# Kernel tuning notes

Measured on AMD Instinct MI355X. Metric: run time of the kernel, lower is better.

Reference implementation:

```python
import jax, jax.numpy as jnp
import numpy as np

B, T = 16, 8192
L, RC, DC, SC, EC, E, NC = 16, 32, 32, 256, 256, 100, 256


def conv1d(x, w, b, dilation=1):
    # x: [B, Cin, T], w: [Cout, Cin, K], b: [Cout]
    y = jax.lax.conv_general_dilated(
        x, w, window_strides=(1,), padding='VALID',
        rhs_dilation=(dilation,), dimension_numbers=('NCH', 'OIH', 'NCH'))
    return y + b[None, :, None]


def setup_inputs() -> dict:
    key = jax.random.key(0)
    ks = jax.random.split(key, 32)
    n = lambda k, shp: (jax.random.normal(k, shp) * 0.1).astype(jnp.float32)
    return dict(
        tokens=jax.random.randint(ks[0], (B, T), 0, NC),
        emb=n(ks[1], (NC, E)),
        init_w=n(ks[2], (RC, E, 1)), init_b=n(ks[3], (RC,)),
        dil_w=n(ks[4], (L, DC, RC, 2)), dil_b=n(ks[5], (L, DC)),
        filt_w=n(ks[6], (L, DC, DC, 2)), filt_b=n(ks[7], (L, DC)),
        gate_w=n(ks[8], (L, DC, DC, 2)), gate_b=n(ks[9], (L, DC)),
        res_w=n(ks[10], (L, RC, DC, 1)), res_b=n(ks[11], (L, RC)),
        skip_w=n(ks[12], (L, SC, DC, 1)), skip_b=n(ks[13], (L, SC)),
        end1_w=n(ks[14], (EC, SC, 1)), end1_b=n(ks[15], (EC,)),
        end2_w=n(ks[16], (EC, EC, 1)), end2_b=n(ks[17], (EC,)),
        fc1_w=n(ks[18], (128, 256)), fc1_b=n(ks[19], (128,)),
        fc2_w=n(ks[20], (128, 128)), fc2_b=n(ks[21], (128,)),
        fc3_w=n(ks[22], (64, 128)), fc3_b=n(ks[23], (64,)),
        fc4_w=n(ks[24], (NC, 64)), fc4_b=n(ks[25], (NC,)),
    )


def reference(tokens, emb, init_w, init_b, dil_w, dil_b, filt_w, filt_b,
              gate_w, gate_b, res_w, res_b, skip_w, skip_b,
              end1_w, end1_b, end2_w, end2_b,
              fc1_w, fc1_b, fc2_w, fc2_b, fc3_w, fc3_b, fc4_w, fc4_b):
    x = emb[tokens]                     # [B, T, E]
    x = jnp.transpose(x, (0, 2, 1))     # [B, E, T]
    x = conv1d(x, init_w, init_b)       # [B, RC, T]
    skip = None
    for i in range(L):
        d = 2 ** (i % 4)                # dilation resets each block of 4 layers
        xp = jnp.pad(x, ((0, 0), (0, 0), (d + 1, 0)))        # left pad d+1
        residual = conv1d(xp, dil_w[i], dil_b[i], dilation=d)  # [B, DC, T+1]
        f = jnp.tanh(conv1d(residual, filt_w[i], filt_b[i]))   # [B, DC, T]
        g = jax.nn.sigmoid(conv1d(residual, gate_w[i], gate_b[i]))
        x = f * g
        skip = conv1d(x, skip_w[i], skip_b[i])   # overwritten each layer (source bug, kept faithful)
        x = conv1d(x, res_w[i], res_b[i]) + residual[:, :, :-1]
    h = jax.nn.relu(conv1d(jax.nn.relu(skip), end1_w, end1_b))
    h = conv1d(h, end2_w, end2_b)       # [B, EC, T]
    h = h[:, :, -1]                     # [B, 256] last timestep only
    h = jax.nn.relu(h @ fc1_w.T + fc1_b)
    h = jax.nn.relu(h @ fc2_w.T + fc2_b)
    h = jax.nn.relu(h @ fc3_w.T + fc3_b)
    out = h @ fc4_w.T + fc4_b           # [B, NC]
    return out
```

## Files before the change

### kernel.cpp

```cpp
#include <hip/hip_runtime.h>


#define BB 16
#define TT 8192
#define LL 16
#define W0 77
#define NT 256

typedef __attribute__((ext_vector_type(8)))  short short8;
typedef __attribute__((ext_vector_type(16))) float float16;

#define MFMA_B16(a, b, c) __builtin_amdgcn_mfma_f32_32x32x16_bf16(a, b, c, 0, 0, 0)

__device__ __forceinline__ short f2bs(float f) {
  union { float ff; unsigned u; } v; v.ff = f;
  unsigned u = v.u;
  return (short)((u + 0x7FFFu + ((u >> 16) & 1u)) >> 16);
}
__device__ __forceinline__ float b2f(short h) {
  union { unsigned u; float f; } v;
  v.u = ((unsigned)(unsigned short)h) << 16; return v.f;
}
__device__ __forceinline__ unsigned cvtpk(float lo, float hi) {
  unsigned r;
  asm("v_cvt_pk_bf16_f32 %0, %1, %2" : "=v"(r) : "v"(lo), "v"(hi));
  return r;
}
__device__ __forceinline__ short8 mk8(unsigned a, unsigned b, unsigned c, unsigned d) {
  union { unsigned u[4]; short8 s; } z;
  z.u[0] = a; z.u[1] = b; z.u[2] = c; z.u[3] = d; return z.s;
}
__device__ __forceinline__ float u2f(unsigned u) {
  union { unsigned x; float f; } z; z.x = u; return z.f;
}
__device__ __forceinline__ void asmb(const unsigned* own, const unsigned* cr,
                                     int kh, unsigned* o) {
  #pragma unroll
  for (int h = 0; h < 2; h++) {
    o[4*h+0] = kh ? cr[4*h+2] : own[4*h+0];
    o[4*h+1] = kh ? cr[4*h+3] : own[4*h+1];
    o[4*h+2] = kh ? own[4*h+2] : cr[4*h+0];
    o[4*h+3] = kh ? own[4*h+3] : cr[4*h+1];
  }
}

__device__ __forceinline__ void afrag2(const short* src, int row, int kh, short8* out) {
  out[0] = *(const short8*)&src[row * 32 + 8 * kh];
  out[1] = *(const short8*)&src[row * 32 + 16 + 8 * kh];
}

__device__ __forceinline__ void ldrow(const short* xb, int row, int kh, unsigned* w8) {
  #pragma unroll
  for (int h = 0; h < 2; h++) {
    short8 v = *(const short8*)&xb[row * 32 + 16 * h + 8 * kh];
    union { short8 s; unsigned u[4]; } z; z.s = v;
    #pragma unroll
    for (int s = 0; s < 4; s++) w8[4 * h + s] = z.u[s];
  }
}

__device__ __forceinline__ void load_chunk(
    int li, int cid, float* pf,
    const float* dil_w, const float* filt_w, const float* gate_w, const float* res_w)
{
  int mat = cid >> 7;
  int h = (cid >> 6) & 1, ln = cid & 63;
  int n = ln & 31, k2 = ln >> 5;
  int base = (li * 32 + n) * 32 + 16 * h + 8 * k2;
  if (mat == 6) {
    const float* p = res_w + base;
    #pragma unroll
    for (int j = 0; j < 8; j++) pf[j] = p[j];
  } else {
    const float* w = (mat < 2) ? dil_w : (mat < 4) ? filt_w : gate_w;
    const float* p = w + base * 2 + (mat & 1);
    #pragma unroll
    for (int j = 0; j < 8; j++) pf[j] = p[2 * j];
  }
}

__global__ __launch_bounds__(NT, 1) void wavenet_kernel(
    const int* __restrict__ tokens,
    const float* __restrict__ emb,
    const float* __restrict__ init_w, const float* __restrict__ init_b,
    const float* __restrict__ dil_w,  const float* __restrict__ dil_b,
    const float* __restrict__ filt_w, const float* __restrict__ filt_b,
    const float* __restrict__ gate_w, const float* __restrict__ gate_b,
    const float* __restrict__ res_w,  const float* __restrict__ res_b,
    const float* __restrict__ skip_w, const float* __restrict__ skip_b,
    const float* __restrict__ end1_w, const float* __restrict__ end1_b,
    const float* __restrict__ end2_w, const float* __restrict__ end2_b,
    const float* __restrict__ fc1_w,  const float* __restrict__ fc1_b,
    const float* __restrict__ fc2_w,  const float* __restrict__ fc2_b,
    const float* __restrict__ fc3_w,  const float* __restrict__ fc3_b,
    const float* __restrict__ fc4_w,  const float* __restrict__ fc4_b,
    float* __restrict__ out)
{
  __shared__ __align__(16) short bfw[2][7168];
  __shared__ __align__(16) float bias2[2][128];
  __shared__ __align__(16) short xbuf[2][W0 * 32];
  __shared__ __align__(16) short pool[8624];
  __shared__ int tok[W0];
  __shared__ __align__(16) float vecA[256], vecB[256];

  short* rb = pool;
  short* xm = pool + 2432;

  const int tid  = threadIdx.x;
  const int lane = tid & 63;
  const int wv   = tid >> 6;
  const int m    = lane & 31;
  const int kh   = lane >> 5;
  const int b    = blockIdx.x;

  if (tid < W0) tok[tid] = tokens[b * TT + (TT - 1 - tid)];
  __syncthreads();

  for (int cid = tid; cid < 77 * 14; cid += NT) {
    int u = cid / 14, s = cid % 14;
    const float* er = emb + tok[u] * 100 + s * 8;
    short8 v;
    if (s < 12) {
      #pragma unroll
      for (int j = 0; j < 8; j++) v[j] = f2bs(er[j]);
    } else if (s == 12) {
      #pragma unroll
      for (int j = 0; j < 4; j++) v[j] = f2bs(er[j]);
      #pragma unroll
      for (int j = 4; j < 8; j++) v[j] = 0;
    } else {
      #pragma unroll
      for (int j = 0; j < 8; j++) v[j] = 0;
    }
    *(short8*)&pool[u * 112 + s * 8] = v;
  }
  for (int cid = tid; cid < 896; cid += NT) {
    float pf[8];
    load_chunk(0, cid, pf, dil_w, filt_w, gate_w, res_w);
    short8 v;
    #pragma unroll
    for (int j = 0; j < 8; j++) v[j] = f2bs(pf[j]);
    *(short8*)&bfw[0][cid * 8] = v;
  }
  if (tid < 128) {
    const float* bsrc = (tid < 32) ? dil_b : (tid < 64) ? filt_b : (tid < 96) ? gate_b : res_b;
    bias2[0][tid] = bsrc[tid & 31];
  }
  __syncthreads();

  if (wv < 3) {
    short8 bi[7];
    #pragma unroll
    for (int s = 0; s < 7; s++) {
      const float* p = init_w + m * 100 + s * 16 + kh * 8;
      short8 v;
      if (s < 6) {
        #pragma unroll
        for (int j = 0; j < 8; j++) v[j] = f2bs(p[j]);
      } else if (kh == 0) {
        #pragma unroll
        for (int j = 0; j < 4; j++) v[j] = f2bs(p[j]);
        #pragma unroll
        for (int j = 4; j < 8; j++) v[j] = 0;
      } else {
        #pragma unroll
        for (int j = 0; j < 8; j++) v[j] = 0;
      }
      bi[s] = v;
    }
    const float binit = init_b[m];
    const int R = wv * 32;
    int u = R + m; if (u > 76) u = 76;
    float16 acc;
    #pragma unroll
    for (int r = 0; r < 16; r++) acc[r] = binit;
    #pragma unroll
    for (int s = 0; s < 7; s++) {
      short8 a = *(const short8*)&pool[u * 112 + s * 16 + kh * 8];
      acc = MFMA_B16(a, bi[s], acc);
    }
    #pragma unroll
    for (int r = 0; r < 16; r++) {
      int row = (r & 3) + 8 * (r >> 2) + 4 * kh;
      int uu = R + row;
      if (uu < W0) xbuf[0][uu * 32 + m] = f2bs(acc[r]);
    }
  }
  __syncthreads();

  int Win = W0;
  for (int i = 0; i < 10; i++) {
    const int d = 1 << (i & 3);
    const int Wout = Win - d - 1;
    const int T = (Wout + 31) / 31;
    const short* bw = bfw[i & 1];
    const float* bs = bias2[i & 1];
    const short* xin  = xbuf[i & 1];
    short* xout = xbuf[(i + 1) & 1];

    float pfo[4][8];
    float pbias = 0.f;
    const int nch = (tid < 128) ? 4 : 3;
    const bool oldpf = (T >= 3) && (i + 1 < LL);
    if (oldpf) {
      #pragma unroll
      for (int q = 0; q < 4; q++) {
        if (q < nch)
          load_chunk(i + 1, tid + q * NT, pfo[q], dil_w, filt_w, gate_w, res_w);
      }
      if (tid < 128) {
        const float* bsrc = (tid < 32) ? dil_b : (tid < 64) ? filt_b : (tid < 96) ? gate_b : res_b;
        pbias = bsrc[(i + 1) * 32 + (tid & 31)];
      }
    }
    const bool newpf = (T <= 2) && (i + 1 < LL) && (wv >= T);
    const int nP = NT - T * 64;
    const int ptid = tid - T * 64;
    float pfn[7][8];
    if (newpf) {
      #pragma unroll
      for (int q = 0; q < 7; q++) {
        int c = ptid + q * nP;
        if (c < 896) load_chunk(i + 1, c, pfn[q], dil_w, filt_w, gate_w, res_w);
      }
    }

    if (wv < T) {
      const int R = wv * 31;
      short8 B0[2], B1[2], BW[5][2];
      #pragma unroll
      for (int h = 0; h < 2; h++) {
        B0[h] = *(const short8*)&bw[((0 * 2 + h) * 64 + lane) * 8];
        B1[h] = *(const short8*)&bw[((1 * 2 + h) * 64 + lane) * 8];
      }
      #pragma unroll
      for (int mt = 0; mt < 5; mt++)
        #pragma unroll
        for (int h = 0; h < 2; h++)
          BW[mt][h] = *(const short8*)&bw[(((mt + 2) * 2 + h) * 64 + lane) * 8];

      int vra = R + m + d; if (vra > Win - 1) vra = Win - 1;
      int vrz = R + m;     if (vrz > Win - 1) vrz = Win - 1;
      short8 aA[2], aZ[2];
      afrag2(xin, vra, kh, aA);
      afrag2(xin, vrz, kh, aZ);
      float16 acc;
      const float bc = bs[m];
      #pragma unroll
      for (int r = 0; r < 16; r++) acc[r] = bc;
      acc = MFMA_B16(aA[0], B0[0], acc);
      acc = MFMA_B16(aA[1], B0[1], acc);
      acc = MFMA_B16(aZ[0], B1[0], acc);
      acc = MFMA_B16(aZ[1], B1[1], acc);
      #pragma unroll
      for (int r = 0; r < 16; r++) {
        int row = (r & 3) + 8 * (r >> 2) + 4 * kh;
        int vr = R + row;
        if (vr <= Wout) rb[vr * 32 + m] = f2bs(acc[r]);
      }
      asm volatile("s_waitcnt lgkmcnt(0)" ::: "memory");

      const int capA = (R + 31 < Wout) ? (R + 31) : Wout;
      int r1 = R + m + 1; if (r1 > capA) r1 = capA;
      int r0 = R + m;     if (r0 > Wout) r0 = Wout;
      short8 a1[2], a0[2];
      afrag2(rb, r1, kh, a1);
      afrag2(rb, r0, kh, a0);
      float16 accF, accG;
      const float bf = bs[32 + m], bg = bs[64 + m];
      #pragma unroll
      for (int r = 0; r < 16; r++) { accF[r] = bf; accG[r] = bg; }
      accF = MFMA_B16(a1[0], BW[0][0], accF);
      accF = MFMA_B16(a1[1], BW[0][1], accF);
      accF = MFMA_B16(a0[0], BW[1][0], accF);
      accF = MFMA_B16(a0[1], BW[1][1], accF);
      accG = MFMA_B16(a1[0], BW[2][0], accG);
      accG = MFMA_B16(a1[1], BW[2][1], accG);
      accG = MFMA_B16(a0[0], BW[3][0], accG);
      accG = MFMA_B16(a0[1], BW[3][1], accG);
      #pragma unroll
      for (int r = 0; r < 16; r++) {
        int row = (r & 3) + 8 * (r >> 2) + 4 * kh;
        int uf = R + row;
        if (row < 31 && uf < Wout) {
          float u = __expf(-2.f * accF[r]);
          float v = __expf(-accG[r]);
          float fg = (1.f - u) * __builtin_amdgcn_rcpf((1.f + u) * (1.f + v));
          xm[uf * 32 + m] = f2bs(fg);
        }
      }
      asm volatile("s_waitcnt lgkmcnt(0)" ::: "memory");

      const int capX = (R + 30 < Wout - 1) ? (R + 30) : (Wout - 1);
      int rx = R + m; if (rx > capX) rx = capX;
      short8 aX[2];
      afrag2(xm, rx, kh, aX);
      float16 accX;
      const float br = bs[96 + m];
      #pragma unroll
      for (int r = 0; r < 16; r++) {
        int row = (r & 3) + 8 * (r >> 2) + 4 * kh;
        int rr = R + row + 1; if (rr > Wout) rr = Wout;
        accX[r] = br + b2f(rb[rr * 32 + m]);
      }
      accX = MFMA_B16(aX[0], BW[4][0], accX);
      accX = MFMA_B16(aX[1], BW[4][1], accX);
      #pragma unroll
      for (int r = 0; r < 16; r++) {
        int row = (r & 3) + 8 * (r >> 2) + 4 * kh;
        int uf = R + row;
        if (row < 31 && uf < Wout) xout[uf * 32 + m] = f2bs(accX[r]);
      }
    } else if (newpf) {
      short* dst = bfw[(i + 1) & 1];
      #pragma unroll
      for (int q = 0; q < 7; q++) {
        int c = ptid + q * nP;
        if (c < 896) {
          short8 v;
          #pragma unroll
          for (int j = 0; j < 8; j++) v[j] = f2bs(pfn[q][j]);
          *(short8*)&dst[c * 8] = v;
        }
      }
      for (int t2 = ptid; t2 < 128; t2 += nP) {
        const float* bsrc = (t2 < 32) ? dil_b : (t2 < 64) ? filt_b : (t2 < 96) ? gate_b : res_b;
        bias2[(i + 1) & 1][t2] = bsrc[(i + 1) * 32 + (t2 & 31)];
      }
    }

    if (oldpf) {
      short* dst = bfw[(i + 1) & 1];
      #pragma unroll
      for (int q = 0; q < 4; q++) {
        if (q < nch) {
          short8 v;
          #pragma unroll
          for (int j = 0; j < 8; j++) v[j] = f2bs(pfo[q][j]);
          *(short8*)&dst[(tid + q * NT) * 8] = v;
        }
      }
      if (tid < 128) bias2[(i + 1) & 1][tid] = pbias;
    }
    __syncthreads();
    Win = Wout;
  }

  {
    const int t31 = lane & 31;
    const int hb  = lane & 32;
    unsigned xcur[8], e32[8], e33[8];
    if (wv == 0) {
      const short* xb0 = xbuf[0];
      int tcl = t31 < Win - 1 ? t31 : Win - 1;
      ldrow(xb0, tcl, kh, xcur);
      ldrow(xb0, 32, kh, e32);
      ldrow(xb0, 33, kh, e33);
    }

    #pragma unroll
    for (int i = 10; i < LL; i++) {
      const int d = 1 << (i & 3);
      const int Wout = Win - d - 1;
      const short* bw = bfw[i & 1];
      const float* bs = bias2[i & 1];

      const bool npf = (i + 1 < LL) && (wv >= 1);
      const int ptid = tid - 64;
      float pfn[7][8];
      if (npf) {
        #pragma unroll
        for (int q = 0; q < 7; q++) {
          int c = ptid + q * 192;
          if (c < 896) load_chunk(i + 1, c, pfn[q], dil_w, filt_w, gate_w, res_w);
        }
      }

      if (wv == 0) {
        short8 WA[7][2];
        #pragma unroll
        for (int mt = 0; mt < 7; mt++)
          #pragma unroll
          for (int h = 0; h < 2; h++)
            WA[mt][h] = *(const short8*)&bw[((mt * 2 + h) * 64 + lane) * 8];

        unsigned xd[8];
        if (i == 10) {
          int td = t31 + d;
          int ts = td > 31 ? 31 : td;
          #pragma unroll
          for (int q = 0; q < 8; q++) {
            unsigned s = (unsigned)__shfl((int)xcur[q], hb | ts);
            s = (td == 32) ? e32[q] : s;
            s = (td >= 33) ? e33[q] : s;
            xd[q] = s;
          }
        } else {
          int td = t31 + d; if (td > Win - 1) td = Win - 1;
          int srcd = hb | td;
          #pragma unroll
          for (int q = 0; q < 8; q++) xd[q] = (unsigned)__shfl((int)xcur[q], srcd);
        }
        float16 acc;
        #pragma unroll
        for (int g = 0; g < 4; g++) {
          float4 b4 = *(const float4*)&bs[4 * kh + 8 * g];
          acc[4*g+0] = b4.x; acc[4*g+1] = b4.y; acc[4*g+2] = b4.z; acc[4*g+3] = b4.w;
        }
        acc = MFMA_B16(WA[0][0], mk8(xd[0], xd[1], xd[2], xd[3]), acc);
        acc = MFMA_B16(WA[0][1], mk8(xd[4], xd[5], xd[6], xd[7]), acc);
        acc = MFMA_B16(WA[1][0], mk8(xcur[0], xcur[1], xcur[2], xcur[3]), acc);
        acc = MFMA_B16(WA[1][1], mk8(xcur[4], xcur[5], xcur[6], xcur[7]), acc);

        unsigned wrb[8], xc[8], x1[8], x1c[8];
        #pragma unroll
        for (int q = 0; q < 8; q++) wrb[q] = cvtpk(acc[2 * q], acc[2 * q + 1]);
        int t1 = t31 + 1; if (t1 > Wout) t1 = Wout;
        int s1o = hb | t1;
        int s1c = (hb ^ 32) | t1;
        #pragma unroll
        for (int q = 0; q < 8; q++) {
          xc[q]  = (unsigned)__shfl((int)wrb[q], lane ^ 32);
          x1[q]  = (unsigned)__shfl((int)wrb[q], s1o);
          x1c[q] = (unsigned)__shfl((int)wrb[q], s1c);
        }
        unsigned rb0w[8], rb1w[8];
        asmb(wrb, xc, kh, rb0w);
        asmb(x1, x1c, kh, rb1w);

        float16 accF, accG;
        #pragma unroll
        for (int g = 0; g < 4; g++) {
          float4 bF = *(const float4*)&bs[32 + 4 * kh + 8 * g];
          float4 bG = *(const float4*)&bs[64 + 4 * kh + 8 * g];
          accF[4*g+0] = bF.x; accF[4*g+1] = bF.y; accF[4*g+2] = bF.z; accF[4*g+3] = bF.w;
          accG[4*g+0] = bG.x; accG[4*g+1] = bG.y; accG[4*g+2] = bG.z; accG[4*g+3] = bG.w;
        }
        short8 RB10 = mk8(rb1w[0], rb1w[1], rb1w[2], rb1w[3]);
        short8 RB11 = mk8(rb1w[4], rb1w[5], rb1w[6], rb1w[7]);
        short8 RB00 = mk8(rb0w[0], rb0w[1], rb0w[2], rb0w[3]);
        short8 RB01 = mk8(rb0w[4], rb0w[5], rb0w[6], rb0w[7]);
        accF = MFMA_B16(WA[2][0], RB10, accF);
        accF = MFMA_B16(WA[2][1], RB11, accF);
        accF = MFMA_B16(WA[3][0], RB00, accF);
        accF = MFMA_B16(WA[3][1], RB01, accF);
        accG = MFMA_B16(WA[4][0], RB10, accG);
        accG = MFMA_B16(WA[4][1], RB11, accG);
        accG = MFMA_B16(WA[5][0], RB00, accG);
        accG = MFMA_B16(WA[5][1], RB01, accG);
        float fg[16];
        #pragma unroll
        for (int r = 0; r < 16; r++) {
          float u = __expf(-2.f * accF[r]);
          float v = __expf(-accG[r]);
          fg[r] = (1.f - u) * __builtin_amdgcn_rcpf((1.f + u) * (1.f + v));
        }
        unsigned wxm[8];
        #pragma unroll
        for (int q = 0; q < 8; q++) wxm[q] = cvtpk(fg[2 * q], fg[2 * q + 1]);

        if (i == LL - 1) {
          if (t31 == 0) {
            #pragma unroll
            for (int q = 0; q < 8; q++) {
              int c0 = (2 * q & 3) + 8 * (q >> 1) + 4 * kh;
              *(unsigned*)&xm[c0] = wxm[q];
            }
          }
        } else {
          unsigned xmc[8];
          #pragma unroll
          for (int q = 0; q < 8; q++) xmc[q] = (unsigned)__shfl((int)wxm[q], lane ^ 32);
          unsigned xmw[8];
          asmb(wxm, xmc, kh, xmw);
          float16 accX;
          #pragma unroll
          for (int g = 0; g < 4; g++) {
            float4 bR = *(const float4*)&bs[96 + 4 * kh + 8 * g];
            #pragma unroll
            for (int j = 0; j < 4; j++) {
              int r = 4 * g + j;
              unsigned w = x1[r >> 1];
              float rv = (r & 1) ? u2f(w & 0xFFFF0000u) : u2f(w << 16);
              accX[r] = ((const float*)&bR)[j] + rv;
            }
          }
          accX = MFMA_B16(WA[6][0], mk8(xmw[0], xmw[1], xmw[2], xmw[3]), accX);
          accX = MFMA_B16(WA[6][1], mk8(xmw[4], xmw[5], xmw[6], xmw[7]), accX);
          unsigned wxn[8], xnc[8];
          #pragma unroll
          for (int q = 0; q < 8; q++) wxn[q] = cvtpk(accX[2 * q], accX[2 * q + 1]);
          #pragma unroll
          for (int q = 0; q < 8; q++) xnc[q] = (unsigned)__shfl((int)wxn[q], lane ^ 32);
          asmb(wxn, xnc, kh, xcur);
        }
      } else if (npf) {
        short* dst = bfw[(i + 1) & 1];
        #pragma unroll
        for (int q = 0; q < 7; q++) {
          int c = ptid + q * 192;
          if (c < 896) {
            short8 v;
            #pragma unroll
            for (int j = 0; j < 8; j++) v[j] = f2bs(pfn[q][j]);
            *(short8*)&dst[c * 8] = v;
          }
        }
        for (int t2 = ptid; t2 < 128; t2 += 192) {
          const float* bsrc = (t2 < 32) ? dil_b : (t2 < 64) ? filt_b : (t2 < 96) ? gate_b : res_b;
          bias2[(i + 1) & 1][t2] = bsrc[(i + 1) * 32 + (t2 & 31)];
        }
      }
      __syncthreads();
      Win = Wout;
    }
  }

  {
    float acc = skip_b[15 * 256 + tid];
    const float* wr = skip_w + (15 * 256 + tid) * 32;
    #pragma unroll
    for (int k = 0; k < 32; k += 4) {
      float4 w = *(const float4*)&wr[k];
      acc += (w.x * b2f(xm[k]) + w.y * b2f(xm[k+1])) + (w.z * b2f(xm[k+2]) + w.w * b2f(xm[k+3]));
    }
    vecA[tid] = fmaxf(acc, 0.f);
  }
  __syncthreads();
  {
    const float* wr = end1_w + tid * 256;
    float a4[4] = {0.f, 0.f, 0.f, 0.f};
    #pragma unroll 8
    for (int k = 0; k < 256; k += 16) {
      #pragma unroll
      for (int q = 0; q < 4; q++) {
        float4 w = *(const float4*)&wr[k + 4 * q];
        float4 a = *(const float4*)&vecA[k + 4 * q];
        a4[q] += (w.x * a.x + w.y * a.y) + (w.z * a.z + w.w * a.w);
      }
    }
    vecB[tid] = fmaxf(end1_b[tid] + (a4[0] + a4[1]) + (a4[2] + a4[3]), 0.f);
  }
  __syncthreads();
  {
    const float* wr = end2_w + tid * 256;
    float a4[4] = {0.f, 0.f, 0.f, 0.f};
    #pragma unroll 8
    for (int k = 0; k < 256; k += 16) {
      #pragma unroll
      for (int q = 0; q < 4; q++) {
        float4 w = *(const float4*)&wr[k + 4 * q];
        float4 a = *(const float4*)&vecB[k + 4 * q];
        a4[q] += (w.x * a.x + w.y * a.y) + (w.z * a.z + w.w * a.w);
      }
    }
    float h2 = end2_b[tid] + (a4[0] + a4[1]) + (a4[2] + a4[3]);
    vecA[tid] = h2;
  }
  __syncthreads();
  if (tid < 128) {
    const float* wr = fc1_w + tid * 256;
    float a4[4] = {0.f, 0.f, 0.f, 0.f};
    #pragma unroll 8
    for (int k = 0; k < 256; k += 16) {
      #pragma unroll
      for (int q = 0; q < 4; q++) {
        float4 w = *(const float4*)&wr[k + 4 * q];
        float4 a = *(const float4*)&vecA[k + 4 * q];
        a4[q] += (w.x * a.x + w.y * a.y) + (w.z * a.z + w.w * a.w);
      }
    }
    vecB[tid] = fmaxf(fc1_b[tid] + (a4[0] + a4[1]) + (a4[2] + a4[3]), 0.f);
  }
  __syncthreads();
  if (tid < 128) {
    const float* wr = fc2_w + tid * 128;
    float a4[4] = {0.f, 0.f, 0.f, 0.f};
    #pragma unroll 4
    for (int k = 0; k < 128; k += 16) {
      #pragma unroll
      for (int q = 0; q < 4; q++) {
        float4 w = *(const float4*)&wr[k + 4 * q];
        float4 a = *(const float4*)&vecB[k + 4 * q];
        a4[q] += (w.x * a.x + w.y * a.y) + (w.z * a.z + w.w * a.w);
      }
    }
    vecA[tid] = fmaxf(fc2_b[tid] + (a4[0] + a4[1]) + (a4[2] + a4[3]), 0.f);
  }
  __syncthreads();
  if (tid < 64) {
    const float* wr = fc3_w + tid * 128;
    float a4[4] = {0.f, 0.f, 0.f, 0.f};
    #pragma unroll 4
    for (int k = 0; k < 128; k += 16) {
      #pragma unroll
      for (int q = 0; q < 4; q++) {
        float4 w = *(const float4*)&wr[k + 4 * q];
        float4 a = *(const float4*)&vecA[k + 4 * q];
        a4[q] += (w.x * a.x + w.y * a.y) + (w.z * a.z + w.w * a.w);
      }
    }
    vecB[tid] = fmaxf(fc3_b[tid] + (a4[0] + a4[1]) + (a4[2] + a4[3]), 0.f);
  }
  __syncthreads();
  {
    const float* wr = fc4_w + tid * 64;
    float a4[4] = {0.f, 0.f, 0.f, 0.f};
    #pragma unroll
    for (int k = 0; k < 64; k += 16) {
      #pragma unroll
      for (int q = 0; q < 4; q++) {
        float4 w = *(const float4*)&wr[k + 4 * q];
        float4 a = *(const float4*)&vecB[k + 4 * q];
        a4[q] += (w.x * a.x + w.y * a.y) + (w.z * a.z + w.w * a.w);
      }
    }
    out[b * 256 + tid] = fc4_b[tid] + (a4[0] + a4[1]) + (a4[2] + a4[3]);
  }
}

extern "C" void kernel_launch(void* const* d_in, const int* in_sizes, int n_in,
                              void* d_out, int out_size, void* d_ws, size_t ws_size,
                              hipStream_t stream) {
  wavenet_kernel<<<BB, NT, 0, stream>>>(
      (const int*)d_in[0],    (const float*)d_in[1],  (const float*)d_in[2],  (const float*)d_in[3],
      (const float*)d_in[4],  (const float*)d_in[5],  (const float*)d_in[6],  (const float*)d_in[7],
      (const float*)d_in[8],  (const float*)d_in[9],  (const float*)d_in[10], (const float*)d_in[11],
      (const float*)d_in[12], (const float*)d_in[13], (const float*)d_in[14], (const float*)d_in[15],
      (const float*)d_in[16], (const float*)d_in[17], (const float*)d_in[18], (const float*)d_in[19],
      (const float*)d_in[20], (const float*)d_in[21], (const float*)d_in[22], (const float*)d_in[23],
      (const float*)d_in[24], (const float*)d_in[25], (float*)d_out);
}
```

Measured before the change: 204.9 us.

## Use permlane32_swap for half-wave exchange and restage weight prefetch to drop barriers

In the single-wave tail layers (10-15), the half-wave data exchanges now use permlane32_swap when a runtime probe confirms its lane semantics, falling back to shuffles otherwise. Fewer shuffles are needed to build the shifted operand. Weight staging is reorganized: layers 11 and 14 are staged together early (14 into the freed pool), the remaining layers are staged ahead of time, and the barriers after layers 14 and 15 are removed, replaced by one sync after the loop. Residual reads in the multi-wave path are hoisted ahead of the gate MFMAs. The aim is to cut cross-lane and barrier latency on the serial tail, at the cost of more staging registers and a reliance on the probe for correctness.

```diff
diff --git a/kernel.cpp b/kernel.cpp
--- a/kernel.cpp
+++ b/kernel.cpp
@@ -9,6 +9,7 @@
 
 typedef __attribute__((ext_vector_type(8)))  short short8;
 typedef __attribute__((ext_vector_type(16))) float float16;
+typedef __attribute__((ext_vector_type(2)))  unsigned uv2;
 
 #define MFMA_B16(a, b, c) __builtin_amdgcn_mfma_f32_32x32x16_bf16(a, b, c, 0, 0, 0)
 
@@ -33,6 +34,7 @@
 __device__ __forceinline__ float u2f(unsigned u) {
   union { unsigned x; float f; } z; z.x = u; return z.f;
 }
+
 __device__ __forceinline__ void asmb(const unsigned* own, const unsigned* cr,
                                      int kh, unsigned* o) {
   #pragma unroll
@@ -41,6 +43,28 @@
     o[4*h+1] = kh ? cr[4*h+3] : own[4*h+1];
     o[4*h+2] = kh ? own[4*h+2] : cr[4*h+0];
     o[4*h+3] = kh ? own[4*h+3] : cr[4*h+1];
+  }
+}
+
+__device__ __forceinline__ void exch(unsigned* o, int kh, int lx32, int mode) {
+  if (mode < 2) {
+    #pragma unroll
+    for (int h = 0; h < 2; h++)
+      #pragma unroll
+      for (int j = 0; j < 2; j++) {
+        unsigned A = o[4*h+j], C = o[4*h+2+j];
+        uv2 r = __builtin_amdgcn_permlane32_swap(A, C, false, false);
+        o[4*h+j]   = (mode == 0) ? r[0] : r[1];
+        o[4*h+2+j] = (mode == 0) ? r[1] : r[0];
+      }
+  } else {
+    unsigned cr[8];
+    #pragma unroll
+    for (int q = 0; q < 8; q++) cr[q] = (unsigned)__shfl((int)o[q], lx32);
+    unsigned t[8];
+    asmb(o, cr, kh, t);
+    #pragma unroll
+    for (int q = 0; q < 8; q++) o[q] = t[q];
   }
 }
 
@@ -76,6 +100,33 @@
     const float* p = w + base * 2 + (mat & 1);
     #pragma unroll
     for (int j = 0; j < 8; j++) pf[j] = p[2 * j];
+  }
+}
+
+__device__ __forceinline__ void stage_layer(
+    int li, int ptid, short* dst, float* bdst,
+    const float* dil_w, const float* filt_w, const float* gate_w, const float* res_w,
+    const float* dil_b, const float* filt_b, const float* gate_b, const float* res_b)
+{
+  float pf[5][8];
+  #pragma unroll
+  for (int q = 0; q < 5; q++) {
+    int c = ptid + q * 192;
+    if (c < 896) load_chunk(li, c, pf[q], dil_w, filt_w, gate_w, res_w);
+  }
+  #pragma unroll
+  for (int q = 0; q < 5; q++) {
+    int c = ptid + q * 192;
+    if (c < 896) {
+      short8 v;
+      #pragma unroll
+      for (int j = 0; j < 8; j++) v[j] = f2bs(pf[q][j]);
+      *(short8*)&dst[c * 8] = v;
+    }
+  }
+  for (int t2 = ptid; t2 < 128; t2 += 192) {
+    const float* bsrc = (t2 < 32) ? dil_b : (t2 < 64) ? filt_b : (t2 < 96) ? gate_b : res_b;
+    bdst[t2] = bsrc[li * 32 + (t2 & 31)];
   }
 }
 
@@ -105,6 +156,8 @@
 
   short* rb = pool;
   short* xm = pool + 2432;
+  short* l14w = pool;
+  float* l14b = (float*)&pool[7168];
 
   const int tid  = threadIdx.x;
   const int lane = tid & 63;
@@ -266,6 +319,13 @@
       short8 a1[2], a0[2];
       afrag2(rb, r1, kh, a1);
       afrag2(rb, r0, kh, a0);
+      float cinit[16];
+      #pragma unroll
+      for (int r = 0; r < 16; r++) {
+        int row = (r & 3) + 8 * (r >> 2) + 4 * kh;
+        int rr = R + row + 1; if (rr > Wout) rr = Wout;
+        cinit[r] = b2f(rb[rr * 32 + m]);
+      }
       float16 accF, accG;
       const float bf = bs[32 + m], bg = bs[64 + m];
       #pragma unroll
@@ -298,11 +358,7 @@
       float16 accX;
       const float br = bs[96 + m];
       #pragma unroll
-      for (int r = 0; r < 16; r++) {
-        int row = (r & 3) + 8 * (r >> 2) + 4 * kh;
-        int rr = R + row + 1; if (rr > Wout) rr = Wout;
-        accX[r] = br + b2f(rb[rr * 32 + m]);
-      }
+      for (int r = 0; r < 16; r++) accX[r] = br + cinit[r];
       accX = MFMA_B16(aX[0], BW[4][0], accX);
       accX = MFMA_B16(aX[1], BW[4][1], accX);
       #pragma unroll
@@ -349,30 +405,74 @@
   {
     const int t31 = lane & 31;
     const int hb  = lane & 32;
+    const int lx32 = lane ^ 32;
     unsigned xcur[8], e32[8], e33[8];
+    int mode = 2;
     if (wv == 0) {
       const short* xb0 = xbuf[0];
       int tcl = t31 < Win - 1 ? t31 : Win - 1;
       ldrow(xb0, tcl, kh, xcur);
       ldrow(xb0, 32, kh, e32);
       ldrow(xb0, 33, kh, e33);
+      {
+        unsigned pa = (unsigned)lane;
+        unsigned pb = 64u + (unsigned)lane;
+        uv2 pr = __builtin_amdgcn_permlane32_swap(pa, pb, false, false);
+        unsigned x0  = (unsigned)__shfl((int)pr[0], 0);
+        unsigned x32 = (unsigned)__shfl((int)pr[0], 32);
+        unsigned y0  = (unsigned)__shfl((int)pr[1], 0);
+        unsigned y32 = (unsigned)__shfl((int)pr[1], 32);
+        if      (x0 == 0u  && x32 == 64u && y0 == 32u && y32 == 96u) mode = 0;
+        else if (y0 == 0u  && y32 == 64u && x0 == 32u && x32 == 96u) mode = 1;
+      }
     }
 
     #pragma unroll
     for (int i = 10; i < LL; i++) {
       const int d = 1 << (i & 3);
       const int Wout = Win - d - 1;
-      const short* bw = bfw[i & 1];
-      const float* bs = bias2[i & 1];
-
-      const bool npf = (i + 1 < LL) && (wv >= 1);
-      const int ptid = tid - 64;
-      float pfn[7][8];
-      if (npf) {
-        #pragma unroll
-        for (int q = 0; q < 7; q++) {
-          int c = ptid + q * 192;
-          if (c < 896) load_chunk(i + 1, c, pfn[q], dil_w, filt_w, gate_w, res_w);
+      const short* bw = (i == 14) ? l14w : (i == 15) ? bfw[0] : bfw[i & 1];
+      const float* bs = (i == 14) ? l14b : (i == 15) ? bias2[0] : bias2[i & 1];
+
+      if (wv >= 1) {
+        const int ptid = tid - 64;
+        if (i == 10) {
+          float pfA[5][8], pfB[5][8];
+          #pragma unroll
+          for (int q = 0; q < 5; q++) {
+            int c = ptid + q * 192;
+            if (c < 896) load_chunk(11, c, pfA[q], dil_w, filt_w, gate_w, res_w);
+          }
+          #pragma unroll
+          for (int q = 0; q < 5; q++) {
+            int c = ptid + q * 192;
+            if (c < 896) load_chunk(14, c, pfB[q], dil_w, filt_w, gate_w, res_w);
+          }
+          #pragma unroll
+          for (int q = 0; q < 5; q++) {
+            int c = ptid + q * 192;
+            if (c < 896) {
+              short8 vA, vB;
+              #pragma unroll
+              for (int j = 0; j < 8; j++) { vA[j] = f2bs(pfA[q][j]); vB[j] = f2bs(pfB[q][j]); }
+              *(short8*)&bfw[1][c * 8] = vA;
+              *(short8*)&l14w[c * 8]   = vB;
+            }
+          }
+          for (int t2 = ptid; t2 < 128; t2 += 192) {
+            const float* bsrc = (t2 < 32) ? dil_b : (t2 < 64) ? filt_b : (t2 < 96) ? gate_b : res_b;
+            bias2[1][t2] = bsrc[11 * 32 + (t2 & 31)];
+            l14b[t2]     = bsrc[14 * 32 + (t2 & 31)];
+          }
+        } else if (i == 11) {
+          stage_layer(12, ptid, bfw[0], bias2[0], dil_w, filt_w, gate_w, res_w,
+                      dil_b, filt_b, gate_b, res_b);
+        } else if (i == 12) {
+          stage_layer(13, ptid, bfw[1], bias2[1], dil_w, filt_w, gate_w, res_w,
+                      dil_b, filt_b, gate_b, res_b);
+        } else if (i == 13) {
+          stage_layer(15, ptid, bfw[0], bias2[0], dil_w, filt_w, gate_w, res_w,
+                      dil_b, filt_b, gate_b, res_b);
         }
       }
 
@@ -407,26 +507,20 @@
           float4 b4 = *(const float4*)&bs[4 * kh + 8 * g];
           acc[4*g+0] = b4.x; acc[4*g+1] = b4.y; acc[4*g+2] = b4.z; acc[4*g+3] = b4.w;
         }
+        acc = MFMA_B16(WA[1][0], mk8(xcur[0], xcur[1], xcur[2], xcur[3]), acc);
+        acc = MFMA_B16(WA[1][1], mk8(xcur[4], xcur[5], xcur[6], xcur[7]), acc);
         acc = MFMA_B16(WA[0][0], mk8(xd[0], xd[1], xd[2], xd[3]), acc);
         acc = MFMA_B16(WA[0][1], mk8(xd[4], xd[5], xd[6], xd[7]), acc);
-        acc = MFMA_B16(WA[1][0], mk8(xcur[0], xcur[1], xcur[2], xcur[3]), acc);
-        acc = MFMA_B16(WA[1][1], mk8(xcur[4], xcur[5], xcur[6], xcur[7]), acc);
-
-        unsigned wrb[8], xc[8], x1[8], x1c[8];
-        #pragma unroll
-        for (int q = 0; q < 8; q++) wrb[q] = cvtpk(acc[2 * q], acc[2 * q + 1]);
+
+        unsigned rb0w[8];
+        #pragma unroll
+        for (int q = 0; q < 8; q++) rb0w[q] = cvtpk(acc[2 * q], acc[2 * q + 1]);
+        exch(rb0w, kh, lx32, mode);
         int t1 = t31 + 1; if (t1 > Wout) t1 = Wout;
         int s1o = hb | t1;
-        int s1c = (hb ^ 32) | t1;
-        #pragma unroll
-        for (int q = 0; q < 8; q++) {
-          xc[q]  = (unsigned)__shfl((int)wrb[q], lane ^ 32);
-          x1[q]  = (unsigned)__shfl((int)wrb[q], s1o);
-          x1c[q] = (unsigned)__shfl((int)wrb[q], s1c);
-        }
-        unsigned rb0w[8], rb1w[8];
-        asmb(wrb, xc, kh, rb0w);
-        asmb(x1, x1c, kh, rb1w);
+        unsigned rb1w[8];
+        #pragma unroll
+        for (int q = 0; q < 8; q++) rb1w[q] = (unsigned)__shfl((int)rb0w[q], s1o);
 
         float16 accF, accG;
         #pragma unroll
@@ -436,18 +530,18 @@
           accF[4*g+0] = bF.x; accF[4*g+1] = bF.y; accF[4*g+2] = bF.z; accF[4*g+3] = bF.w;
           accG[4*g+0] = bG.x; accG[4*g+1] = bG.y; accG[4*g+2] = bG.z; accG[4*g+3] = bG.w;
         }
+        short8 RB00 = mk8(rb0w[0], rb0w[1], rb0w[2], rb0w[3]);
+        short8 RB01 = mk8(rb0w[4], rb0w[5], rb0w[6], rb0w[7]);
         short8 RB10 = mk8(rb1w[0], rb1w[1], rb1w[2], rb1w[3]);
         short8 RB11 = mk8(rb1w[4], rb1w[5], rb1w[6], rb1w[7]);
-        short8 RB00 = mk8(rb0w[0], rb0w[1], rb0w[2], rb0w[3]);
-        short8 RB01 = mk8(rb0w[4], rb0w[5], rb0w[6], rb0w[7]);
+        accF = MFMA_B16(WA[3][0], RB00, accF);
+        accF = MFMA_B16(WA[3][1], RB01, accF);
         accF = MFMA_B16(WA[2][0], RB10, accF);
         accF = MFMA_B16(WA[2][1], RB11, accF);
-        accF = MFMA_B16(WA[3][0], RB00, accF);
-        accF = MFMA_B16(WA[3][1], RB01, accF);
+        accG = MFMA_B16(WA[5][0], RB00, accG);
+        accG = MFMA_B16(WA[5][1], RB01, accG);
         accG = MFMA_B16(WA[4][0], RB10, accG);
         accG = MFMA_B16(WA[4][1], RB11, accG);
-        accG = MFMA_B16(WA[5][0], RB00, accG);
-        accG = MFMA_B16(WA[5][1], RB01, accG);
         float fg[16];
         #pragma unroll
         for (int r = 0; r < 16; r++) {
@@ -464,15 +558,18 @@
             #pragma unroll
             for (int q = 0; q < 8; q++) {
               int c0 = (2 * q & 3) + 8 * (q >> 1) + 4 * kh;
-              *(unsigned*)&xm[c0] = wxm[q];
+              *(unsigned*)&xbuf[0][c0] = wxm[q];
             }
           }
         } else {
-          unsigned xmc[8];
-          #pragma unroll
-          for (int q = 0; q < 8; q++) xmc[q] = (unsigned)__shfl((int)wxm[q], lane ^ 32);
+          unsigned x1[8];
+          #pragma unroll
+          for (int q = 0; q < 8; q++) x1[q] = rb1w[q];
+          exch(x1, kh, lx32, mode);
           unsigned xmw[8];
-          asmb(wxm, xmc, kh, xmw);
+          #pragma unroll
+          for (int q = 0; q < 8; q++) xmw[q] = wxm[q];
+          exch(xmw, kh, lx32, mode);
           float16 accX;
           #pragma unroll
           for (int g = 0; g < 4; g++) {
@@ -487,42 +584,25 @@
           }
           accX = MFMA_B16(WA[6][0], mk8(xmw[0], xmw[1], xmw[2], xmw[3]), accX);
           accX = MFMA_B16(WA[6][1], mk8(xmw[4], xmw[5], xmw[6], xmw[7]), accX);
-          unsigned wxn[8], xnc[8];
-          #pragma unroll
-          for (int q = 0; q < 8; q++) wxn[q] = cvtpk(accX[2 * q], accX[2 * q + 1]);
-          #pragma unroll
-          for (int q = 0; q < 8; q++) xnc[q] = (unsigned)__shfl((int)wxn[q], lane ^ 32);
-          asmb(wxn, xnc, kh, xcur);
-        }
-      } else if (npf) {
-        short* dst = bfw[(i + 1) & 1];
-        #pragma unroll
-        for (int q = 0; q < 7; q++) {
-          int c = ptid + q * 192;
-          if (c < 896) {
-            short8 v;
-            #pragma unroll
-            for (int j = 0; j < 8; j++) v[j] = f2bs(pfn[q][j]);
-            *(short8*)&dst[c * 8] = v;
-          }
-        }
-        for (int t2 = ptid; t2 < 128; t2 += 192) {
-          const float* bsrc = (t2 < 32) ? dil_b : (t2 < 64) ? filt_b : (t2 < 96) ? gate_b : res_b;
-          bias2[(i + 1) & 1][t2] = bsrc[(i + 1) * 32 + (t2 & 31)];
-        }
-      }
-      __syncthreads();
+          #pragma unroll
+          for (int q = 0; q < 8; q++) xcur[q] = cvtpk(accX[2 * q], accX[2 * q + 1]);
+          exch(xcur, kh, lx32, mode);
+        }
+      }
+      if (i <= 13) __syncthreads();
       Win = Wout;
     }
   }
+  __syncthreads();
 
   {
+    const short* xmt = xbuf[0];
     float acc = skip_b[15 * 256 + tid];
     const float* wr = skip_w + (15 * 256 + tid) * 32;
     #pragma unroll
     for (int k = 0; k < 32; k += 4) {
       float4 w = *(const float4*)&wr[k];
-      acc += (w.x * b2f(xm[k]) + w.y * b2f(xm[k+1])) + (w.z * b2f(xm[k+2]) + w.w * b2f(xm[k+3]));
+      acc += (w.x * b2f(xmt[k]) + w.y * b2f(xmt[k+1])) + (w.z * b2f(xmt[k+2]) + w.w * b2f(xmt[k+3]));
     }
     vecA[tid] = fmaxf(acc, 0.f);
   }
```

Measured after the change: 203.5 us. About the same (-0.7%).
